# Optimization experiments

Hardware: AMD Instinct MI355X
Metric: run time of the kernel (lower is better)

Reference implementation:

```python
import jax, jax.numpy as jnp
import numpy as np

B, L, D = 4, 4096, 1024
H = 16
DK = D // H  # 64
EPS = 1e-5


def setup_inputs() -> dict:
    key = jax.random.key(0)
    ks = jax.random.split(key, 9)
    s = 1.0 / np.sqrt(D)
    return {
        "Q": jax.random.normal(ks[0], (B, L, D), dtype=jnp.float32),
        "W_Q": jax.random.uniform(ks[1], (D, D), jnp.float32, -s, s),
        "b_Q": jax.random.uniform(ks[2], (D,), jnp.float32, -s, s),
        "W_K": jax.random.uniform(ks[3], (D, D), jnp.float32, -s, s),
        "b_K": jax.random.uniform(ks[4], (D,), jnp.float32, -s, s),
        "W_V": jax.random.uniform(ks[5], (D, D), jnp.float32, -s, s),
        "b_V": jax.random.uniform(ks[6], (D,), jnp.float32, -s, s),
        "W_O": jax.random.uniform(ks[7], (D, D), jnp.float32, -s, s),
        "b_O": jax.random.uniform(ks[8], (D,), jnp.float32, -s, s),
    }


def reference(Q, W_Q, b_Q, W_K, b_K, W_V, b_V, W_O, b_O):
    # Projections (torch Linear: x @ W.T + b). K = V = Q (self-attention).
    q = (Q @ W_Q.T + b_Q).reshape(B, L, H, DK)  # blhd
    k = (Q @ W_K.T + b_K).reshape(B, L, H, DK)
    v = (Q @ W_V.T + b_V).reshape(B, L, H, DK)

    phi_q = jax.nn.elu(q) + 1.0
    phi_k = jax.nn.elu(k) + 1.0

    # KV outer-product accumulation over sequence: [b,h,d,m]
    KV = jnp.einsum('blhd,blhm->bhdm', phi_k, v)
    K_sum = phi_k.sum(axis=1)                       # [b,h,d]
    Z = 1.0 / (jnp.einsum('blhd,bhd->blh', phi_q, K_sum) + EPS)
    V_new = jnp.einsum('blhd,bhdm->blhm', phi_q, KV) * Z[..., None]

    out = V_new.reshape(B, L, H * DK) @ W_O.T + b_O  # [b,L,d_model]
    return out
```

## Files before the change

kernel.cpp:

```cpp
#include <hip/hip_runtime.h>

typedef unsigned short u16;
typedef unsigned int   u32;
typedef __attribute__((ext_vector_type(8))) short short8;
typedef __attribute__((ext_vector_type(4))) float f32x4;
typedef __attribute__((ext_vector_type(4))) u16   u16x4;

#define NB 4
#define SL 4096
#define DM 1024
#define NH 16
#define DK 64

__device__ __forceinline__ u16 f2bf(float f) {
  u32 u = __builtin_bit_cast(u32, f);
  u = (u + 0x7fffu + ((u >> 16) & 1u)) >> 16;
  return (u16)u;
}
__device__ __forceinline__ float bf2f(u16 v) {
  u32 u = ((u32)v) << 16;
  return __builtin_bit_cast(float, u);
}
__device__ __forceinline__ float eluP1(float x) {
  return x > 0.f ? x + 1.f : __expf(x);
}
#define GLL(gp, lp) __builtin_amdgcn_global_load_lds(     \
    (const __attribute__((address_space(1))) void*)(gp),  \
    (__attribute__((address_space(3))) void*)(lp), 16, 0, 0)

__global__ void cvt_all(const float* __restrict__ Qf,
                        const float* __restrict__ WQ, const float* __restrict__ WK,
                        const float* __restrict__ WV, const float* __restrict__ WO,
                        const float* __restrict__ bQ, const float* __restrict__ bK,
                        const float* __restrict__ bV,
                        u16* __restrict__ Qbf, u16* __restrict__ Wqkv,
                        u16* __restrict__ Wobf, float* __restrict__ biasQKV) {
  int b = blockIdx.x, tid = threadIdx.x;
  if (b < 16384) {
    int i = b * 256 + tid;
    f32x4 f = *(const f32x4*)(Qf + (size_t)i * 4);
    u16x4 o = { f2bf(f[0]), f2bf(f[1]), f2bf(f[2]), f2bf(f[3]) };
    *(u16x4*)(Qbf + (size_t)i * 4) = o;
  } else if (b < 20480) {
    int r = (b - 16384) >> 10;
    int i = ((b - 16384) & 1023) * 256 + tid;
    const float* src = r == 0 ? WQ : r == 1 ? WK : r == 2 ? WV : WO;
    u16* dst = (r == 3) ? Wobf : Wqkv + (size_t)r * 1048576;
    f32x4 f = *(const f32x4*)(src + (size_t)i * 4);
    u16x4 o = { f2bf(f[0]), f2bf(f[1]), f2bf(f[2]), f2bf(f[3]) };
    *(u16x4*)(dst + (size_t)i * 4) = o;
  } else {
    int i = (b - 20480) * 256 + tid;
    if (i < 3072) {
      float v = (i < 1024) ? bQ[i] : (i < 2048) ? bK[i - 1024] : bV[i - 2048];
      biasQKV[i] = v;
    }
  }
}

#define COMPUTE(CB)                                                          \
  do {                                                                       \
    short8 af_[4], bf_[4];                                                   \
    _Pragma("unroll") for (int t = 0; t < 4; t++)                            \
        af_[t] = *(const short8*)(aP[t] + (CB));                             \
    _Pragma("unroll") for (int u = 0; u < 4; u++)                            \
        bf_[u] = *(const short8*)(bP[u] + (CB));                             \
    _Pragma("unroll") for (int t = 0; t < 4; t++)                            \
      _Pragma("unroll") for (int u = 0; u < 4; u++)                          \
          acc[t][u] = __builtin_amdgcn_mfma_f32_16x16x32_bf16(               \
              af_[t], bf_[u], acc[t][u], 0, 0, 0);                           \
  } while (0)

#define STAGE4(XB, WB)                                        \
  do {                                                        \
    GLL(Ag0, XB); GLL(Ag1, (XB) + 512);                       \
    GLL(Wg0, WB); GLL(Wg1, (WB) + 512);                       \
    Ag0 += 32; Ag1 += 32; Wg0 += 32; Wg1 += 32;               \
  } while (0)

__global__ __launch_bounds__(256) void gemm_qkv(const u16* __restrict__ A,
                                                const u16* __restrict__ Wqkv,
                                                const float* __restrict__ biasQKV,
                                                u16* __restrict__ phiq,
                                                u16* __restrict__ phiKT,
                                                u16* __restrict__ vT) {
  const int K = 1024;
  const int bId = blockIdx.x;
  const int xcd = bId & 7, s = bId >> 3;
  const int xm = xcd >> 1, xn = xcd & 1;
  const int tm_l = s / 12, tn_l = s - tm_l * 12;
  const int tile_m = xm * 32 + tm_l;
  const int tile_n = xn * 12 + tn_l;
  const int region = tile_n >> 3;

  const int tid = threadIdx.x, lane = tid & 63, wv = tid >> 6;
  const int i16 = lane & 15, q = lane >> 4;
  const int waveR = wv >> 1, waveC = wv & 1;

  __shared__ u16 smem[16384];

  const int rbase = wv * 32 + (lane >> 2);
  const int kc = (lane & 3) ^ ((rbase >> 1) & 3);
  const u16* Ag0 = A + (size_t)(tile_m * 128 + rbase) * K + kc * 8;
  const u16* Ag1 = Ag0 + 16 * K;
  const u16* Wg0 = Wqkv + (size_t)(tile_n * 128 + rbase) * K + kc * 8;
  const u16* Wg1 = Wg0 + 16 * K;
  u16* X0 = smem + wv * 1024;
  u16* W0 = smem + 4096 + wv * 1024;
  u16* X1 = X0 + 8192;
  u16* W1 = W0 + 8192;

  const u16* aT0 = (region == 0) ? smem + 4096 : smem;
  const u16* bT0 = (region == 0) ? smem : smem + 4096;
  const u16* aP[4];
  const u16* bP[4];
#pragma unroll
  for (int t = 0; t < 4; t++) {
    int m = waveR * 64 + t * 16 + i16;
    aP[t] = aT0 + m * 32 + ((q ^ ((m >> 1) & 3)) << 3);
  }
#pragma unroll
  for (int u = 0; u < 4; u++) {
    int m = waveC * 64 + u * 16 + i16;
    bP[u] = bT0 + m * 32 + ((q ^ ((m >> 1) & 3)) << 3);
  }

  f32x4 acc[4][4] = {};

  STAGE4(X0, W0);

  for (int kk = 0; kk < 16; kk++) {
    __syncthreads();
    STAGE4(X1, W1);
    COMPUTE(0);
    __syncthreads();
    if (kk < 15) STAGE4(X0, W0);
    COMPUTE(8192);
  }

  u16* T = smem;
  u16* dstT = (region == 1) ? phiKT : vT;
#pragma unroll
  for (int h = 0; h < 2; h++) {
    __syncthreads();
    if (waveR == h) {
#pragma unroll
      for (int t = 0; t < 4; t++) {
#pragma unroll
        for (int u = 0; u < 4; u++) {
          int cI = waveC * 64 + u * 16 + i16;
          int rI = t * 16 + q * 4;
          u16x4 o;
          if (region == 0) {
            f32x4 b4 = *(const f32x4*)(biasQKV + tile_n * 128 + h * 64 + rI);
#pragma unroll
            for (int r = 0; r < 4; r++) o[r] = f2bf(eluP1(acc[t][u][r] + b4[r]));
          } else {
            float bs = biasQKV[tile_n * 128 + cI];
#pragma unroll
            for (int r = 0; r < 4; r++) {
              float vv = acc[t][u][r] + bs;
              if (region == 1) vv = eluP1(vv);
              o[r] = f2bf(vv);
            }
          }
          *(u16x4*)(T + cI * 72 + rI) = o;
        }
      }
    }
    __syncthreads();
    const int Rl = tid >> 3, j = tid & 7;
#pragma unroll
    for (int p = 0; p < 4; p++) {
      int R = p * 32 + Rl;
      short8 v8 = *(const short8*)(T + R * 72 + j * 8);
      if (region == 0) {
        *(short8*)(phiq + (size_t)(tile_m * 128 + R) * DM + tile_n * 128 + h * 64 + j * 8) = v8;
      } else {
        int n_loc = tile_n * 128 + R - region * 1024;
        int bI = tile_m >> 5;
        int l = (tile_m & 31) * 128 + h * 64 + j * 8;
        *(short8*)(dstT + ((size_t)bI * 1024 + n_loc) * 4096 + l) = v8;
      }
    }
  }
}

__global__ __launch_bounds__(256) void gemm_out(const u16* __restrict__ A,
                                                const u16* __restrict__ W,
                                                const float* __restrict__ bias,
                                                float* __restrict__ outp) {
  const int K = 1024;
  const int bId = blockIdx.x;
  const int xcd = bId & 7, s = bId >> 3;
  const int xm = xcd >> 1, xn = xcd & 1;
  const int tm_l = s >> 2, tn_l = s & 3;
  const int tile_m = xm * 32 + tm_l;
  const int tile_n = xn * 4 + tn_l;

  const int tid = threadIdx.x, lane = tid & 63, wv = tid >> 6;
  const int i16 = lane & 15, q = lane >> 4;
  const int waveR = wv >> 1, waveC = wv & 1;

  __shared__ u16 smem[17408];

  const int rbase = wv * 32 + (lane >> 2);
  const int kc = (lane & 3) ^ ((rbase >> 1) & 3);
  const u16* Ag0 = A + (size_t)(tile_m * 128 + rbase) * K + kc * 8;
  const u16* Ag1 = Ag0 + 16 * K;
  const u16* Wg0 = W + (size_t)(tile_n * 128 + rbase) * K + kc * 8;
  const u16* Wg1 = Wg0 + 16 * K;
  u16* X0 = smem + wv * 1024;
  u16* W0 = smem + 4096 + wv * 1024;
  u16* X1 = X0 + 8192;
  u16* W1 = W0 + 8192;

  const u16* aP[4];
  const u16* bP[4];
#pragma unroll
  for (int t = 0; t < 4; t++) {
    int m = waveR * 64 + t * 16 + i16;
    aP[t] = smem + 4096 + m * 32 + ((q ^ ((m >> 1) & 3)) << 3);
  }
#pragma unroll
  for (int u = 0; u < 4; u++) {
    int m = waveC * 64 + u * 16 + i16;
    bP[u] = smem + m * 32 + ((q ^ ((m >> 1) & 3)) << 3);
  }

  f32x4 acc[4][4] = {};

  STAGE4(X0, W0);

  for (int kk = 0; kk < 16; kk++) {
    __syncthreads();
    STAGE4(X1, W1);
    COMPUTE(0);
    __syncthreads();
    if (kk < 15) STAGE4(X0, W0);
    COMPUTE(8192);
  }

  float* Tf = (float*)smem;
#pragma unroll
  for (int half = 0; half < 2; half++) {
    __syncthreads();
    if (waveR == half) {
#pragma unroll
      for (int t = 0; t < 4; t++) {
#pragma unroll
        for (int u = 0; u < 4; u++) {
          int cI = waveC * 64 + u * 16 + i16;
          int rIh = t * 16 + q * 4;
          f32x4 b4 = *(const f32x4*)(bias + tile_n * 128 + half * 64 + rIh);
          f32x4 o;
#pragma unroll
          for (int r = 0; r < 4; r++) o[r] = acc[t][u][r] + b4[r];
          *(f32x4*)(Tf + cI * 68 + rIh) = o;
        }
      }
    }
    __syncthreads();
    const int Rl = tid >> 4, j = tid & 15;
#pragma unroll
    for (int p = 0; p < 8; p++) {
      int R = p * 16 + Rl;
      f32x4 v = *(const f32x4*)(Tf + R * 68 + j * 4);
      *(f32x4*)(outp + (size_t)(tile_m * 128 + R) * DM + tile_n * 128 + half * 64 + j * 4) = v;
    }
  }
}

__global__ __launch_bounds__(256) void kv_partial(const u16* __restrict__ phiKT,
                                                  const u16* __restrict__ vT,
                                                  float* __restrict__ part,
                                                  float* __restrict__ ksumP) {
  int bh = blockIdx.x >> 2, chunk = blockIdx.x & 3;
  int tid = threadIdx.x, lane = tid & 63, wv = tid >> 6;
  int i16 = lane & 15, q = lane >> 4;
  const u16* Ab = phiKT + (size_t)bh * DK * SL;
  const u16* Bb = vT + (size_t)bh * DK * SL;
  int l0 = (chunk * 4 + wv) * 256;
  f32x4 acc[4][4] = {};
  float ks[4] = {};
  for (int kk = 0; kk < 256; kk += 32) {
    int col = l0 + kk + q * 8;
    short8 af[4], bfr[4];
#pragma unroll
    for (int t = 0; t < 4; t++) af[t] = *(const short8*)(Ab + (size_t)(t * 16 + i16) * SL + col);
#pragma unroll
    for (int u = 0; u < 4; u++) bfr[u] = *(const short8*)(Bb + (size_t)(u * 16 + i16) * SL + col);
#pragma unroll
    for (int t = 0; t < 4; t++)
#pragma unroll
      for (int j = 0; j < 8; j++) ks[t] += bf2f((u16)af[t][j]);
#pragma unroll
    for (int t = 0; t < 4; t++)
#pragma unroll
      for (int u = 0; u < 4; u++)
        acc[t][u] = __builtin_amdgcn_mfma_f32_16x16x32_bf16(af[t], bfr[u], acc[t][u], 0, 0, 0);
  }
  __shared__ float red[4][64][64];
  __shared__ float ksl[4][4][64];
#pragma unroll
  for (int t = 0; t < 4; t++)
#pragma unroll
    for (int u = 0; u < 4; u++)
#pragma unroll
      for (int r = 0; r < 4; r++)
        red[wv][t * 16 + q * 4 + r][u * 16 + i16] = acc[t][u][r];
#pragma unroll
  for (int t = 0; t < 4; t++) ksl[wv][q][t * 16 + i16] = ks[t];
  __syncthreads();
  int d = tid >> 2, mg = (tid & 3) * 16;
#pragma unroll
  for (int c = 0; c < 4; c++) {
    int m = mg + c * 4;
    f32x4 o;
#pragma unroll
    for (int r = 0; r < 4; r++)
      o[r] = red[0][d][m + r] + red[1][d][m + r] + red[2][d][m + r] + red[3][d][m + r];
    *(f32x4*)(part + ((size_t)(chunk * 64 + bh) * 64 + d) * 64 + m) = o;
  }
  if (tid < 64) {
    float s = 0.f;
#pragma unroll
    for (int w2 = 0; w2 < 4; w2++)
#pragma unroll
      for (int q2 = 0; q2 < 4; q2++) s += ksl[w2][q2][tid];
    ksumP[chunk * 4096 + bh * 64 + tid] = s;
  }
}

__global__ __launch_bounds__(256) void kv_finalize(const float* __restrict__ part,
                                                   const float* __restrict__ ksumP,
                                                   u16* __restrict__ KVt,
                                                   float* __restrict__ Ksum) {
  int bh = blockIdx.x, tid = threadIdx.x;
  for (int e = tid; e < 4096; e += 256) {
    int d = e >> 6, m = e & 63;
    float s = part[((size_t)(0 * 64 + bh) * 64 + d) * 64 + m]
            + part[((size_t)(1 * 64 + bh) * 64 + d) * 64 + m]
            + part[((size_t)(2 * 64 + bh) * 64 + d) * 64 + m]
            + part[((size_t)(3 * 64 + bh) * 64 + d) * 64 + m];
    KVt[(size_t)bh * 4096 + m * 64 + d] = f2bf(s);
  }
  if (tid < 64) {
    float s = ksumP[0 * 4096 + bh * 64 + tid] + ksumP[1 * 4096 + bh * 64 + tid]
            + ksumP[2 * 4096 + bh * 64 + tid] + ksumP[3 * 4096 + bh * 64 + tid];
    Ksum[bh * 64 + tid] = s;
  }
}

__global__ __launch_bounds__(256) void vnew_kernel(const u16* __restrict__ phiq,
                                                   const u16* __restrict__ KVt,
                                                   const float* __restrict__ Ksum,
                                                   u16* __restrict__ Vnew) {
  int bh = blockIdx.x >> 5, lt = blockIdx.x & 31;
  int b = bh >> 4, h = bh & 15;
  int tid = threadIdx.x, lane = tid & 63, wv = tid >> 6;
  int i16 = lane & 15, q = lane >> 4;
  int waveM = wv & 1, waveL = wv >> 1;

  __shared__ float Zs[128];
  __shared__ float Pp[128][2];
  __shared__ u16 T[128 * 72];
  {
    int l = tid >> 1, half = tid & 1;
    const u16* pr = phiq + (size_t)(b * SL + lt * 128 + l) * DM + h * 64 + half * 32;
    float s = 0.f;
    for (int i = 0; i < 32; i += 8) {
      short8 v8 = *(const short8*)(pr + i);
#pragma unroll
      for (int j = 0; j < 8; j++) s += bf2f((u16)v8[j]) * Ksum[bh * 64 + half * 32 + i + j];
    }
    Pp[l][half] = s;
  }
  __syncthreads();
  if (tid < 128) Zs[tid] = 1.0f / (Pp[tid][0] + Pp[tid][1] + 1e-5f);
  __syncthreads();

  f32x4 acc[2][4] = {};
#pragma unroll
  for (int step = 0; step < 2; step++) {
    int d0 = step * 32 + q * 8;
    short8 af[2], bfr[4];
#pragma unroll
    for (int t = 0; t < 2; t++) {
      int m = waveM * 32 + t * 16 + i16;
      af[t] = *(const short8*)(KVt + (size_t)bh * 4096 + m * 64 + d0);
    }
#pragma unroll
    for (int u = 0; u < 4; u++) {
      int l = lt * 128 + waveL * 64 + u * 16 + i16;
      bfr[u] = *(const short8*)(phiq + (size_t)(b * SL + l) * DM + h * 64 + d0);
    }
#pragma unroll
    for (int t = 0; t < 2; t++)
#pragma unroll
      for (int u = 0; u < 4; u++)
        acc[t][u] = __builtin_amdgcn_mfma_f32_16x16x32_bf16(af[t], bfr[u], acc[t][u], 0, 0, 0);
  }

#pragma unroll
  for (int t = 0; t < 2; t++) {
#pragma unroll
    for (int u = 0; u < 4; u++) {
      int cI = waveL * 64 + u * 16 + i16;
      int nI = waveM * 32 + t * 16 + q * 4;
      float z = Zs[cI];
      u16x4 o;
#pragma unroll
      for (int r = 0; r < 4; r++) o[r] = f2bf(acc[t][u][r] * z);
      *(u16x4*)(T + cI * 72 + nI) = o;
    }
  }
  __syncthreads();
  {
    const int Rl = tid >> 3, j = tid & 7;
#pragma unroll
    for (int p = 0; p < 4; p++) {
      int R = p * 32 + Rl;
      short8 v8 = *(const short8*)(T + R * 72 + j * 8);
      *(short8*)(Vnew + (size_t)(b * SL + lt * 128 + R) * DM + h * 64 + j * 8) = v8;
    }
  }
}

extern "C" void kernel_launch(void* const* d_in, const int* in_sizes, int n_in,
                              void* d_out, int out_size, void* d_ws, size_t ws_size,
                              hipStream_t stream) {
  const float* Qf = (const float*)d_in[0];
  const float* WQ = (const float*)d_in[1];
  const float* bQ = (const float*)d_in[2];
  const float* WK = (const float*)d_in[3];
  const float* bK = (const float*)d_in[4];
  const float* WV = (const float*)d_in[5];
  const float* bV = (const float*)d_in[6];
  const float* WO = (const float*)d_in[7];
  const float* bO = (const float*)d_in[8];

  const size_t MB = 1024ull * 1024ull;
  char* ws = (char*)d_ws;
  u16* Qbf     = (u16*)(ws + 0);
  u16* Vnew    = (u16*)(ws + 0);
  u16* Wqkv    = (u16*)(ws + 32 * MB);
  u16* Wobf    = (u16*)(ws + 38 * MB);
  float* biasQKV = (float*)(ws + 40 * MB);
  u16* phiq    = (u16*)(ws + 41 * MB);
  u16* phiKT   = (u16*)(ws + 73 * MB);
  u16* vT      = (u16*)(ws + 105 * MB);
  u16* KVt     = (u16*)(ws + 137 * MB);
  float* Ksum  = (float*)(ws + 138 * MB);
  float* part  = (float*)(ws + 139 * MB);
  float* ksumP = (float*)(ws + 143 * MB);

  cvt_all<<<20492, 256, 0, stream>>>(Qf, WQ, WK, WV, WO, bQ, bK, bV,
                                     Qbf, Wqkv, Wobf, biasQKV);

  gemm_qkv<<<3072, 256, 0, stream>>>(Qbf, Wqkv, biasQKV, phiq, phiKT, vT);

  kv_partial<<<256, 256, 0, stream>>>(phiKT, vT, part, ksumP);
  kv_finalize<<<64, 256, 0, stream>>>(part, ksumP, KVt, Ksum);

  vnew_kernel<<<2048, 256, 0, stream>>>(phiq, KVt, Ksum, Vnew);

  gemm_out<<<1024, 256, 0, stream>>>(Vnew, Wobf, bO, (float*)d_out);
}
```

Baseline: 366.5 us.

## Rewrite QKV GEMM with 256x256 tiles, 8 waves and phased LDS pipeline

The QKV projection GEMM now uses 256x256 output tiles with 512 threads (8 waves, each computing 128x64), which raises data reuse per global load. It replaces the two-stage __syncthreads loop with a finer-grained schedule: K is split into 32-wide sub-stages with async global-to-LDS loads issued between MFMA phases, explicit vmcnt waits, raw s_barrier and s_setprio around the MFMA bursts. The grid mapping changes so each XCD owns a band of M tiles. The goal is to hide memory latency and cut barrier stalls, at the cost of 128KB of LDS per block and higher register pressure, which limits occupancy and makes the hand-ordered waits fragile.

```diff
diff --git a/kernel.cpp b/kernel.cpp
--- a/kernel.cpp
+++ b/kernel.cpp
@@ -58,6 +58,169 @@
   }
 }
 
+
+#define VM6 asm volatile("s_waitcnt vmcnt(6)" ::: "memory")
+#define NOP ((void)0)
+
+#define SA(buf, ks, kt) do {                                      \
+    const u16* g_ = Ag + (((kt) & 15) * 64 + (ks) * 32);          \
+    u16* l_ = ldsA + (buf) * 32768 + (ks) * 8192;                 \
+    GLL(g_, l_); GLL(g_ + 16 * 1024, l_ + 512); } while (0)
+
+#define SB(buf, ks, kt) do {                                      \
+    const u16* g_ = Wg + (((kt) & 15) * 64 + (ks) * 32);          \
+    u16* l_ = ldsB + (buf) * 32768 + (ks) * 8192;                 \
+    GLL(g_, l_); GLL(g_ + 16 * 1024, l_ + 512); } while (0)
+
+#define LDB(buf, ks) do {                                         \
+    const u16* pB_ = bBase + (buf) * 32768 + (ks) * 8192;         \
+    bf0 = *(const short8*)(pB_ + bOff[0]);                        \
+    bf1 = *(const short8*)(pB_ + bOff[1]);                        \
+    bf2 = *(const short8*)(pB_ + bOff[2]);                        \
+    bf3 = *(const short8*)(pB_ + bOff[3]); } while (0)
+
+#define PHASE(buf, ks, tb, PRE, STG, WT) do {                     \
+    short8 af_[4];                                                \
+    const u16* pA_ = aBase + (buf) * 32768 + (ks) * 8192;         \
+    _Pragma("unroll") for (int t_ = 0; t_ < 4; t_++)              \
+      af_[t_] = *(const short8*)(pA_ + aOff[(tb) + t_]);          \
+    PRE;                                                          \
+    STG;                                                          \
+    WT;                                                           \
+    __builtin_amdgcn_s_barrier();                                 \
+    asm volatile("s_waitcnt lgkmcnt(0)" ::: "memory");            \
+    __builtin_amdgcn_s_setprio(1);                                \
+    _Pragma("unroll") for (int t_ = 0; t_ < 4; t_++) {            \
+      acc[(tb) + t_][0] = __builtin_amdgcn_mfma_f32_16x16x32_bf16(af_[t_], bf0, acc[(tb) + t_][0], 0, 0, 0); \
+      acc[(tb) + t_][1] = __builtin_amdgcn_mfma_f32_16x16x32_bf16(af_[t_], bf1, acc[(tb) + t_][1], 0, 0, 0); \
+      acc[(tb) + t_][2] = __builtin_amdgcn_mfma_f32_16x16x32_bf16(af_[t_], bf2, acc[(tb) + t_][2], 0, 0, 0); \
+      acc[(tb) + t_][3] = __builtin_amdgcn_mfma_f32_16x16x32_bf16(af_[t_], bf3, acc[(tb) + t_][3], 0, 0, 0); \
+    }                                                             \
+    __builtin_amdgcn_s_setprio(0);                                \
+    __builtin_amdgcn_s_barrier();                                 \
+  } while (0)
+
+__global__ __launch_bounds__(512, 2) void gemm_qkv(const u16* __restrict__ A,
+                                                   const u16* __restrict__ Wqkv,
+                                                   const float* __restrict__ biasQKV,
+                                                   u16* __restrict__ phiq,
+                                                   u16* __restrict__ phiKT,
+                                                   u16* __restrict__ vT) {
+  const int K = 1024;
+  const int bId = blockIdx.x;
+  const int xcd = bId & 7, s = bId >> 3;
+  const int tile_m = xcd * 8 + s / 12;
+  const int tile_n = s % 12;
+  const int region = tile_n >> 2;
+
+  const int tid = threadIdx.x, lane = tid & 63, wv = tid >> 6;
+  const int i16 = lane & 15, q = lane >> 4;
+  const int waveM = wv >> 2, waveN = wv & 3;
+
+  __shared__ u16 smem[65536];
+
+  const int r0 = wv * 32 + (lane >> 2);
+  const int kc = (lane & 3) ^ ((r0 >> 1) & 3);
+  const u16* Ag = A + (size_t)(tile_m * 256 + r0) * K + kc * 8;
+  const u16* Wg = Wqkv + (size_t)(tile_n * 256 + r0) * K + kc * 8;
+  u16* ldsA = smem + wv * 1024;
+  u16* ldsB = smem + 16384 + wv * 1024;
+
+  const u16* aBase = (region == 0) ? smem + 16384 : smem;
+  const u16* bBase = (region == 0) ? smem : smem + 16384;
+  int aOff[8], bOff[4];
+#pragma unroll
+  for (int t = 0; t < 8; t++) {
+    int m = waveM * 128 + t * 16 + i16;
+    aOff[t] = m * 32 + ((q ^ ((m >> 1) & 3)) << 3);
+  }
+#pragma unroll
+  for (int u = 0; u < 4; u++) {
+    int n = waveN * 64 + u * 16 + i16;
+    bOff[u] = n * 32 + ((q ^ ((n >> 1) & 3)) << 3);
+  }
+
+  f32x4 acc[8][4] = {};
+  short8 bf0, bf1, bf2, bf3;
+
+  SB(0, 0, 0); SA(0, 0, 0); SB(0, 1, 0); SA(0, 1, 0);
+  SB(1, 0, 1); SA(1, 0, 1); SB(1, 1, 1);
+  VM6;
+  __builtin_amdgcn_s_barrier();
+  asm volatile("" ::: "memory");
+
+#pragma unroll 1
+  for (int i = 0; i < 8; i++) {
+    PHASE(0, 0, 0, LDB(0, 0), SA(1, 1, 2 * i + 1), NOP);
+    PHASE(0, 0, 4, NOP,       SB(0, 0, 2 * i + 2), NOP);
+    PHASE(0, 1, 0, LDB(0, 1), SA(0, 0, 2 * i + 2), NOP);
+    PHASE(0, 1, 4, NOP,       SB(0, 1, 2 * i + 2), VM6);
+    PHASE(1, 0, 0, LDB(1, 0), SA(0, 1, 2 * i + 2), NOP);
+    PHASE(1, 0, 4, NOP,       SB(1, 0, 2 * i + 3), NOP);
+    PHASE(1, 1, 0, LDB(1, 1), SA(1, 0, 2 * i + 3), NOP);
+    PHASE(1, 1, 4, NOP,       SB(1, 1, 2 * i + 3), VM6);
+  }
+
+  u16* T = smem;
+  const int TS = 132;
+  u16* dstT = (region == 1) ? phiKT : vT;
+  const int bI = tile_m >> 4;
+  const int lb = (tile_m & 15) * 256;
+
+#pragma unroll
+  for (int h = 0; h < 2; h++) {
+    __syncthreads();
+    if (waveM == h) {
+      if (region == 0) {
+#pragma unroll
+        for (int t = 0; t < 8; t++) {
+          f32x4 b4 = *(const f32x4*)(biasQKV + tile_n * 256 + h * 128 + t * 16 + q * 4);
+#pragma unroll
+          for (int u = 0; u < 4; u++) {
+            int cC = waveN * 64 + u * 16 + i16;
+            u16x4 o;
+#pragma unroll
+            for (int r = 0; r < 4; r++) o[r] = f2bf(eluP1(acc[t][u][r] + b4[r]));
+            *(u16x4*)(T + cC * TS + t * 16 + q * 4) = o;
+          }
+        }
+      } else {
+#pragma unroll
+        for (int u = 0; u < 4; u++) {
+          int cC = waveN * 64 + u * 16 + i16;
+          float bs = biasQKV[tile_n * 256 + cC];
+#pragma unroll
+          for (int t = 0; t < 8; t++) {
+            u16x4 o;
+#pragma unroll
+            for (int r = 0; r < 4; r++) {
+              float vv = acc[t][u][r] + bs;
+              if (region == 1) vv = eluP1(vv);
+              o[r] = f2bf(vv);
+            }
+            *(u16x4*)(T + cC * TS + t * 16 + q * 4) = o;
+          }
+        }
+      }
+    }
+    __syncthreads();
+    {
+      const int Rl = tid >> 4, c16 = (tid & 15) * 8;
+#pragma unroll
+      for (int p = 0; p < 8; p++) {
+        int R = p * 32 + Rl;
+        short8 v8 = *(const short8*)(T + R * TS + c16);
+        if (region == 0) {
+          *(short8*)(phiq + (size_t)(tile_m * 256 + R) * DM + tile_n * 256 + h * 128 + c16) = v8;
+        } else {
+          int n_loc = tile_n * 256 + R - region * 1024;
+          *(short8*)(dstT + ((size_t)bI * 1024 + n_loc) * 4096 + lb + h * 128 + c16) = v8;
+        }
+      }
+    }
+  }
+}
+
 #define COMPUTE(CB)                                                          \
   do {                                                                       \
     short8 af_[4], bf_[4];                                                   \
@@ -77,114 +240,6 @@
     GLL(Wg0, WB); GLL(Wg1, (WB) + 512);                       \
     Ag0 += 32; Ag1 += 32; Wg0 += 32; Wg1 += 32;               \
   } while (0)
-
-__global__ __launch_bounds__(256) void gemm_qkv(const u16* __restrict__ A,
-                                                const u16* __restrict__ Wqkv,
-                                                const float* __restrict__ biasQKV,
-                                                u16* __restrict__ phiq,
-                                                u16* __restrict__ phiKT,
-                                                u16* __restrict__ vT) {
-  const int K = 1024;
-  const int bId = blockIdx.x;
-  const int xcd = bId & 7, s = bId >> 3;
-  const int xm = xcd >> 1, xn = xcd & 1;
-  const int tm_l = s / 12, tn_l = s - tm_l * 12;
-  const int tile_m = xm * 32 + tm_l;
-  const int tile_n = xn * 12 + tn_l;
-  const int region = tile_n >> 3;
-
-  const int tid = threadIdx.x, lane = tid & 63, wv = tid >> 6;
-  const int i16 = lane & 15, q = lane >> 4;
-  const int waveR = wv >> 1, waveC = wv & 1;
-
-  __shared__ u16 smem[16384];
-
-  const int rbase = wv * 32 + (lane >> 2);
-  const int kc = (lane & 3) ^ ((rbase >> 1) & 3);
-  const u16* Ag0 = A + (size_t)(tile_m * 128 + rbase) * K + kc * 8;
-  const u16* Ag1 = Ag0 + 16 * K;
-  const u16* Wg0 = Wqkv + (size_t)(tile_n * 128 + rbase) * K + kc * 8;
-  const u16* Wg1 = Wg0 + 16 * K;
-  u16* X0 = smem + wv * 1024;
-  u16* W0 = smem + 4096 + wv * 1024;
-  u16* X1 = X0 + 8192;
-  u16* W1 = W0 + 8192;
-
-  const u16* aT0 = (region == 0) ? smem + 4096 : smem;
-  const u16* bT0 = (region == 0) ? smem : smem + 4096;
-  const u16* aP[4];
-  const u16* bP[4];
-#pragma unroll
-  for (int t = 0; t < 4; t++) {
-    int m = waveR * 64 + t * 16 + i16;
-    aP[t] = aT0 + m * 32 + ((q ^ ((m >> 1) & 3)) << 3);
-  }
-#pragma unroll
-  for (int u = 0; u < 4; u++) {
-    int m = waveC * 64 + u * 16 + i16;
-    bP[u] = bT0 + m * 32 + ((q ^ ((m >> 1) & 3)) << 3);
-  }
-
-  f32x4 acc[4][4] = {};
-
-  STAGE4(X0, W0);
-
-  for (int kk = 0; kk < 16; kk++) {
-    __syncthreads();
-    STAGE4(X1, W1);
-    COMPUTE(0);
-    __syncthreads();
-    if (kk < 15) STAGE4(X0, W0);
-    COMPUTE(8192);
-  }
-
-  u16* T = smem;
-  u16* dstT = (region == 1) ? phiKT : vT;
-#pragma unroll
-  for (int h = 0; h < 2; h++) {
-    __syncthreads();
-    if (waveR == h) {
-#pragma unroll
-      for (int t = 0; t < 4; t++) {
-#pragma unroll
-        for (int u = 0; u < 4; u++) {
-          int cI = waveC * 64 + u * 16 + i16;
-          int rI = t * 16 + q * 4;
-          u16x4 o;
-          if (region == 0) {
-            f32x4 b4 = *(const f32x4*)(biasQKV + tile_n * 128 + h * 64 + rI);
-#pragma unroll
-            for (int r = 0; r < 4; r++) o[r] = f2bf(eluP1(acc[t][u][r] + b4[r]));
-          } else {
-            float bs = biasQKV[tile_n * 128 + cI];
-#pragma unroll
-            for (int r = 0; r < 4; r++) {
-              float vv = acc[t][u][r] + bs;
-              if (region == 1) vv = eluP1(vv);
-              o[r] = f2bf(vv);
-            }
-          }
-          *(u16x4*)(T + cI * 72 + rI) = o;
-        }
-      }
-    }
-    __syncthreads();
-    const int Rl = tid >> 3, j = tid & 7;
-#pragma unroll
-    for (int p = 0; p < 4; p++) {
-      int R = p * 32 + Rl;
-      short8 v8 = *(const short8*)(T + R * 72 + j * 8);
-      if (region == 0) {
-        *(short8*)(phiq + (size_t)(tile_m * 128 + R) * DM + tile_n * 128 + h * 64 + j * 8) = v8;
-      } else {
-        int n_loc = tile_n * 128 + R - region * 1024;
-        int bI = tile_m >> 5;
-        int l = (tile_m & 31) * 128 + h * 64 + j * 8;
-        *(short8*)(dstT + ((size_t)bI * 1024 + n_loc) * 4096 + l) = v8;
-      }
-    }
-  }
-}
 
 __global__ __launch_bounds__(256) void gemm_out(const u16* __restrict__ A,
                                                 const u16* __restrict__ W,
@@ -458,7 +513,7 @@
   cvt_all<<<20492, 256, 0, stream>>>(Qf, WQ, WK, WV, WO, bQ, bK, bV,
                                      Qbf, Wqkv, Wobf, biasQKV);
 
-  gemm_qkv<<<3072, 256, 0, stream>>>(Qbf, Wqkv, biasQKV, phiq, phiKT, vT);
+  gemm_qkv<<<768, 512, 0, stream>>>(Qbf, Wqkv, biasQKV, phiq, phiKT, vT);
 
   kv_partial<<<256, 256, 0, stream>>>(phiKT, vT, part, ksumP);
   kv_finalize<<<64, 256, 0, stream>>>(part, ksumP, KVt, Ksum);
```

New measurement: 344.7 us. 1.06x faster.
